# Performance work log

Measured on AMD Instinct MI355X. Metric: run time of the kernel, lower is better.

Reference implementation:

```python
import jax, jax.numpy as jnp
import numpy as np

C = 1024
H = 64
W = 64


def _conv1x1(x, Wt, b):
    # x: [1, Cin, H, W], Wt: [Cout, Cin] -> [1, Cout, H, W]
    return jnp.einsum('oc,bchw->bohw', Wt, x) + b[None, :, None, None]


def setup_inputs() -> dict:
    key = jax.random.key(0)
    ks = jax.random.split(key, 12)
    sc = 1.0 / np.sqrt(C)
    return {
        'x_f': jax.random.normal(ks[0], (1, C, H, W), jnp.float32),
        'x_m': jax.random.normal(ks[1], (1, C, H, W), jnp.float32),
        'x_l': jax.random.normal(ks[2], (1, C, H, W), jnp.float32),
        'Wq': jax.random.normal(ks[3], (C // 2, C), jnp.float32) * sc,
        'bq': jax.random.normal(ks[4], (C // 2,), jnp.float32) * sc,
        'Wk1': jax.random.normal(ks[5], (C // 2, C), jnp.float32) * sc,
        'bk1': jax.random.normal(ks[6], (C // 2,), jnp.float32) * sc,
        'Wk2': jax.random.normal(ks[7], (C // 2, C), jnp.float32) * sc,
        'bk2': jax.random.normal(ks[8], (C // 2,), jnp.float32) * sc,
        'Wv': jax.random.normal(ks[9], (C, C), jnp.float32) * sc,
        'bv': jax.random.normal(ks[10], (C,), jnp.float32) * sc,
        'gamma': jax.random.normal(ks[11], (1,), jnp.float32),
    }


def reference(x_f, x_m, x_l, Wq, bq, Wk1, bk1, Wk2, bk2, Wv, bv, gamma):
    c = x_f.shape[1]
    h, w = x_f.shape[2], x_f.shape[3]
    # torch .view(1, C, -1) on a [1, C/2, H, W] tensor: row-major reshape to [C, H*W/2]
    q = _conv1x1(x_m, Wq, bq).reshape(c, -1).T      # [HW/2, C]
    kf = _conv1x1(x_f, Wk1, bk1).reshape(c, -1)     # [C, HW/2]
    kl = _conv1x1(x_l, Wk2, bk2).reshape(c, -1)     # [C, HW/2]
    att_f = jax.nn.softmax(kf @ q, axis=-1)         # [C, C]
    att_l = jax.nn.softmax(kl @ q, axis=-1)         # [C, C]
    v = _conv1x1(x_m, Wv, bv).reshape(c, -1)        # [C, HW]
    out = att_f @ v + att_l @ v                     # [C, HW]
    out = out.reshape(1, c, h, w)
    return gamma * out + (x_l + x_f) / 2
```

## Files before the change

kernel.cpp:

```cpp
#include <hip/hip_runtime.h>
#include <math.h>


typedef __attribute__((ext_vector_type(8))) short    bf16x8;
typedef __attribute__((ext_vector_type(4))) float    f32x4;

__device__ __forceinline__ unsigned short f2bf(float x) {
    unsigned u = __float_as_uint(x);
    u += 0x7FFFu + ((u >> 16) & 1u);
    return (unsigned short)(u >> 16);
}
__device__ __forceinline__ float bf2f(unsigned short h) {
    return __uint_as_float(((unsigned)h) << 16);
}
__device__ __forceinline__ void split2(float x, unsigned short& h, unsigned short& l) {
    h = f2bf(x);
    l = f2bf(x - bf2f(h));
}

__global__ __launch_bounds__(256) void weights_split_k(
    const float* __restrict__ Wq, const float* __restrict__ Wk1,
    const float* __restrict__ Wk2, const float* __restrict__ Wv,
    unsigned short* __restrict__ Wqh, unsigned short* __restrict__ Wql,
    unsigned short* __restrict__ Wk1h, unsigned short* __restrict__ Wk1l,
    unsigned short* __restrict__ Wk2h, unsigned short* __restrict__ Wk2l,
    unsigned short* __restrict__ Wvh, unsigned short* __restrict__ Wvl)
{
    const int gi = blockIdx.x;
    const float* src; unsigned short *H, *L; int base;
    if (gi < 512)       { src = Wq;  H = Wqh;  L = Wql;  base = gi; }
    else if (gi < 1024) { src = Wk1; H = Wk1h; L = Wk1l; base = gi - 512; }
    else if (gi < 1536) { src = Wk2; H = Wk2h; L = Wk2l; base = gi - 1024; }
    else                { src = Wv;  H = Wvh;  L = Wvl;  base = gi - 1536; }
    const size_t i = (size_t)base * 1024 + threadIdx.x * 4;
    const float4 v = *(const float4*)(src + i);
    ushort4 h, l;
    split2(v.x, h.x, l.x); split2(v.y, h.y, l.y);
    split2(v.z, h.z, l.z); split2(v.w, h.w, l.w);
    *(ushort4*)(H + i) = h;
    *(ushort4*)(L + i) = l;
}

__global__ __launch_bounds__(256) void transpose3_k(
    const float* __restrict__ x0, const float* __restrict__ x1,
    const float* __restrict__ x2,
    unsigned short* __restrict__ t0h, unsigned short* __restrict__ t0l,
    unsigned short* __restrict__ t1h, unsigned short* __restrict__ t1l,
    unsigned short* __restrict__ t2h, unsigned short* __restrict__ t2l)
{
    const float* X; unsigned short *Th, *Tl;
    if (blockIdx.z == 0)      { X = x0; Th = t0h; Tl = t0l; }
    else if (blockIdx.z == 1) { X = x1; Th = t1h; Tl = t1l; }
    else                      { X = x2; Th = t2h; Tl = t2l; }

    __shared__ float t[32 * 33];
    const int tid = threadIdx.x;
    const int c0 = blockIdx.y * 32;
    const int p0 = blockIdx.x * 32;

    const int cl = tid >> 3;
    const int p4 = (tid & 7) * 4;
    const float4 v = *(const float4*)(X + (size_t)(c0 + cl) * 4096 + p0 + p4);
    t[(p4 + 0) * 33 + cl] = v.x;
    t[(p4 + 1) * 33 + cl] = v.y;
    t[(p4 + 2) * 33 + cl] = v.z;
    t[(p4 + 3) * 33 + cl] = v.w;
    __syncthreads();

    const int pl = tid >> 3;
    const int c4 = (tid & 7) * 4;
    ushort4 h, l;
    split2(t[pl * 33 + c4 + 0], h.x, l.x);
    split2(t[pl * 33 + c4 + 1], h.y, l.y);
    split2(t[pl * 33 + c4 + 2], h.z, l.z);
    split2(t[pl * 33 + c4 + 3], h.w, l.w);
    const size_t o = (size_t)(p0 + pl) * 1024 + c0 + c4;
    *(ushort4*)(Th + o) = h;
    *(ushort4*)(Tl + o) = l;
}

__global__ __launch_bounds__(256) void transpose1_k(
    const float* __restrict__ X,
    unsigned short* __restrict__ Th, unsigned short* __restrict__ Tl)
{
    __shared__ float t[32 * 33];
    const int tid = threadIdx.x;
    const int c0 = blockIdx.y * 32;
    const int p0 = blockIdx.x * 32;

    const int cl = tid >> 3;
    const int p4 = (tid & 7) * 4;
    const float4 v = *(const float4*)(X + (size_t)(c0 + cl) * 4096 + p0 + p4);
    t[(p4 + 0) * 33 + cl] = v.x;
    t[(p4 + 1) * 33 + cl] = v.y;
    t[(p4 + 2) * 33 + cl] = v.z;
    t[(p4 + 3) * 33 + cl] = v.w;
    __syncthreads();

    const int pl = tid >> 3;
    const int c4 = (tid & 7) * 4;
    ushort4 h, l;
    split2(t[pl * 33 + c4 + 0], h.x, l.x);
    split2(t[pl * 33 + c4 + 1], h.y, l.y);
    split2(t[pl * 33 + c4 + 2], h.z, l.z);
    split2(t[pl * 33 + c4 + 3], h.w, l.w);
    const size_t o = (size_t)(p0 + pl) * 1024 + c0 + c4;
    *(ushort4*)(Th + o) = h;
    *(ushort4*)(Tl + o) = l;
}

__device__ __forceinline__ void gemm_core(
    const unsigned short* __restrict__ Ah, const unsigned short* __restrict__ Al,
    const unsigned short* __restrict__ Bh, const unsigned short* __restrict__ Bl,
    int ldk, int kbeg, int kend, int m0, int n0,
    unsigned short* As_h, unsigned short* As_l,
    unsigned short* Bs_h, unsigned short* Bs_l,
    f32x4 (&acc)[4][4])
{
    const int tid  = threadIdx.x;
    const int lane = tid & 63;
    const int wv   = tid >> 6;
    const int wm   = (wv >> 1) * 64;
    const int wn   = (wv & 1) * 64;
    const int lr   = lane & 15;
    const int quad = lane >> 4;
    const int r0 = tid >> 2;
    const int sg = (tid & 3) * 8;

    for (int k0 = kbeg; k0 < kend; k0 += 32) {
        const size_t ka = (size_t)(m0 + r0) * ldk + k0 + sg;
        const size_t kb = (size_t)(n0 + r0) * ldk + k0 + sg;
        const bf16x8 a0h = *(const bf16x8*)(Ah + ka);
        const bf16x8 a1h = *(const bf16x8*)(Ah + ka + (size_t)64 * ldk);
        const bf16x8 a0l = *(const bf16x8*)(Al + ka);
        const bf16x8 a1l = *(const bf16x8*)(Al + ka + (size_t)64 * ldk);
        const bf16x8 b0h = *(const bf16x8*)(Bh + kb);
        const bf16x8 b1h = *(const bf16x8*)(Bh + kb + (size_t)64 * ldk);
        const bf16x8 b0l = *(const bf16x8*)(Bl + kb);
        const bf16x8 b1l = *(const bf16x8*)(Bl + kb + (size_t)64 * ldk);

        __syncthreads();
        *(bf16x8*)(As_h + r0 * 40 + sg)        = a0h;
        *(bf16x8*)(As_h + (r0 + 64) * 40 + sg) = a1h;
        *(bf16x8*)(As_l + r0 * 40 + sg)        = a0l;
        *(bf16x8*)(As_l + (r0 + 64) * 40 + sg) = a1l;
        *(bf16x8*)(Bs_h + r0 * 40 + sg)        = b0h;
        *(bf16x8*)(Bs_h + (r0 + 64) * 40 + sg) = b1h;
        *(bf16x8*)(Bs_l + r0 * 40 + sg)        = b0l;
        *(bf16x8*)(Bs_l + (r0 + 64) * 40 + sg) = b1l;
        __syncthreads();

        bf16x8 afh[4], afl[4], bfh[4], bfl[4];
#pragma unroll
        for (int i = 0; i < 4; ++i) {
            const int ra = (wm + i * 16 + lr) * 40 + quad * 8;
            afh[i] = *(const bf16x8*)(As_h + ra);
            afl[i] = *(const bf16x8*)(As_l + ra);
            const int rb = (wn + i * 16 + lr) * 40 + quad * 8;
            bfh[i] = *(const bf16x8*)(Bs_h + rb);
            bfl[i] = *(const bf16x8*)(Bs_l + rb);
        }
#pragma unroll
        for (int i = 0; i < 4; ++i)
#pragma unroll
            for (int j = 0; j < 4; ++j) {
                acc[i][j] = __builtin_amdgcn_mfma_f32_16x16x32_bf16(afh[i], bfh[j], acc[i][j], 0, 0, 0);
                acc[i][j] = __builtin_amdgcn_mfma_f32_16x16x32_bf16(afh[i], bfl[j], acc[i][j], 0, 0, 0);
                acc[i][j] = __builtin_amdgcn_mfma_f32_16x16x32_bf16(afl[i], bfh[j], acc[i][j], 0, 0, 0);
            }
    }
}

#define GEMM_PROLOGUE()                                                 \
    __shared__ unsigned short As_h[128 * 40], As_l[128 * 40];           \
    __shared__ unsigned short Bs_h[128 * 40], Bs_l[128 * 40];           \
    f32x4 acc[4][4];                                                    \
    _Pragma("unroll") for (int i = 0; i < 4; ++i)                       \
    _Pragma("unroll") for (int j = 0; j < 4; ++j)                       \
    _Pragma("unroll") for (int r = 0; r < 4; ++r) acc[i][j][r] = 0.f;   \
    const int lane = threadIdx.x & 63;                                  \
    const int wv   = threadIdx.x >> 6;                                  \
    const int wm   = (wv >> 1) * 64;                                    \
    const int wn   = (wv & 1) * 64;                                     \
    const int lr   = lane & 15;                                         \
    const int quad = lane >> 4;

__global__ __launch_bounds__(256) void conv_all_k(
    const unsigned short* __restrict__ Wqh, const unsigned short* __restrict__ Wql,
    const unsigned short* __restrict__ Wk1h, const unsigned short* __restrict__ Wk1l,
    const unsigned short* __restrict__ Wk2h, const unsigned short* __restrict__ Wk2l,
    const unsigned short* __restrict__ Wvh, const unsigned short* __restrict__ Wvl,
    const unsigned short* __restrict__ xmTh, const unsigned short* __restrict__ xmTl,
    const unsigned short* __restrict__ xfTh, const unsigned short* __restrict__ xfTl,
    const unsigned short* __restrict__ xlTh, const unsigned short* __restrict__ xlTl,
    const float* __restrict__ bq, const float* __restrict__ bk1,
    const float* __restrict__ bk2, const float* __restrict__ bv,
    unsigned short* __restrict__ Qh, unsigned short* __restrict__ Ql,
    unsigned short* __restrict__ Kfh, unsigned short* __restrict__ Kfl,
    unsigned short* __restrict__ Klh, unsigned short* __restrict__ Kll,
    float* __restrict__ V)
{
    GEMM_PROLOGUE();
    const int mt = blockIdx.y;
    const unsigned short *Ah, *Al, *Bh, *Bl;
    const float* bias;
    unsigned short *Ch = nullptr, *Cl = nullptr;
    float* Cv = nullptr;
    int mloc;
    if (mt < 4) {
        Ah = Wqh;  Al = Wql;  Bh = xmTh; Bl = xmTl; bias = bq;
        Ch = Qh;   Cl = Ql;   mloc = mt * 128;
    } else if (mt < 8) {
        Ah = Wk1h; Al = Wk1l; Bh = xfTh; Bl = xfTl; bias = bk1;
        Ch = Kfh;  Cl = Kfl;  mloc = (mt - 4) * 128;
    } else if (mt < 12) {
        Ah = Wk2h; Al = Wk2l; Bh = xlTh; Bl = xlTl; bias = bk2;
        Ch = Klh;  Cl = Kll;  mloc = (mt - 8) * 128;
    } else {
        Ah = Wvh;  Al = Wvl;  Bh = xmTh; Bl = xmTl; bias = bv;
        Cv = V;    mloc = (mt - 12) * 128;
    }
    const int n0 = blockIdx.x * 128;

    gemm_core(Ah, Al, Bh, Bl, 1024, 0, 1024, mloc, n0, As_h, As_l, Bs_h, Bs_l, acc);

#pragma unroll
    for (int i = 0; i < 4; ++i) {
        const int mb = mloc + wm + i * 16 + quad * 4;
#pragma unroll
        for (int j = 0; j < 4; ++j) {
            const int nn = n0 + wn + j * 16 + lr;
#pragma unroll
            for (int r = 0; r < 4; ++r) {
                const float v = acc[i][j][r] + bias[mb + r];
                const size_t idx = (size_t)(mb + r) * 4096 + nn;
                if (Cv) {
                    Cv[idx] = v;
                } else {
                    unsigned short h, l;
                    split2(v, h, l);
                    Ch[idx] = h;
                    Cl[idx] = l;
                }
            }
        }
    }
}

__global__ __launch_bounds__(256) void logits_fused_k(
    const unsigned short* __restrict__ Kfh, const unsigned short* __restrict__ Kfl,
    const unsigned short* __restrict__ Klh, const unsigned short* __restrict__ Kll,
    const unsigned short* __restrict__ Qh, const unsigned short* __restrict__ Ql,
    float* __restrict__ Sfp, float* __restrict__ Slp)
{
    GEMM_PROLOGUE();
    const int which = blockIdx.z >> 2;
    const int slice = blockIdx.z & 3;
    const unsigned short* Ah = which ? Klh : Kfh;
    const unsigned short* Al = which ? Kll : Kfl;
    float* out = (which ? Slp : Sfp) + (size_t)slice * 1024 * 1024;
    const int m0 = blockIdx.y * 128;
    const int n0 = blockIdx.x * 128;

    gemm_core(Ah, Al, Qh, Ql, 2048, slice * 512, slice * 512 + 512, m0, n0,
              As_h, As_l, Bs_h, Bs_l, acc);

#pragma unroll
    for (int i = 0; i < 4; ++i) {
        const int mb = m0 + wm + i * 16 + quad * 4;
#pragma unroll
        for (int j = 0; j < 4; ++j) {
            const int nn = n0 + wn + j * 16 + lr;
#pragma unroll
            for (int r = 0; r < 4; ++r)
                out[(size_t)(mb + r) * 1024 + nn] = acc[i][j][r];
        }
    }
}

__global__ __launch_bounds__(256) void gemm_final_k(
    const unsigned short* __restrict__ Amh, const unsigned short* __restrict__ Aml,
    const unsigned short* __restrict__ VTh, const unsigned short* __restrict__ VTl,
    float* __restrict__ out,
    const float* __restrict__ xf, const float* __restrict__ xl,
    const float* __restrict__ gamma)
{
    GEMM_PROLOGUE();
    const int m0 = blockIdx.y * 128;
    const int n0 = blockIdx.x * 128;

    gemm_core(Amh, Aml, VTh, VTl, 1024, 0, 1024, m0, n0,
              As_h, As_l, Bs_h, Bs_l, acc);

    const float g = gamma[0];
#pragma unroll
    for (int i = 0; i < 4; ++i) {
        const int mb = m0 + wm + i * 16 + quad * 4;
#pragma unroll
        for (int j = 0; j < 4; ++j) {
            const int nn = n0 + wn + j * 16 + lr;
#pragma unroll
            for (int r = 0; r < 4; ++r) {
                const size_t idx = (size_t)(mb + r) * 4096 + nn;
                out[idx] = g * acc[i][j][r] + 0.5f * (xf[idx] + xl[idx]);
            }
        }
    }
}

__global__ __launch_bounds__(256) void softmax_add4_k(
    const float* __restrict__ Sfp, const float* __restrict__ Slp,
    unsigned short* __restrict__ Ah, unsigned short* __restrict__ Al)
{
    const int row = blockIdx.x;
    const int tid = threadIdx.x;
    __shared__ float red[8];
    const size_t base = (size_t)row * 1024 + tid * 4;
    const size_t SL = (size_t)1024 * 1024;

    float4 vf = *(const float4*)(Sfp + base);
    float4 vl = *(const float4*)(Slp + base);
#pragma unroll
    for (int s = 1; s < 4; ++s) {
        const float4 a = *(const float4*)(Sfp + s * SL + base);
        const float4 b = *(const float4*)(Slp + s * SL + base);
        vf.x += a.x; vf.y += a.y; vf.z += a.z; vf.w += a.w;
        vl.x += b.x; vl.y += b.y; vl.z += b.z; vl.w += b.w;
    }

    float mf = fmaxf(fmaxf(vf.x, vf.y), fmaxf(vf.z, vf.w));
    float ml = fmaxf(fmaxf(vl.x, vl.y), fmaxf(vl.z, vl.w));
#pragma unroll
    for (int off = 32; off; off >>= 1) {
        mf = fmaxf(mf, __shfl_down(mf, off, 64));
        ml = fmaxf(ml, __shfl_down(ml, off, 64));
    }
    const int wave = tid >> 6;
    if ((tid & 63) == 0) { red[wave] = mf; red[4 + wave] = ml; }
    __syncthreads();
    mf = fmaxf(fmaxf(red[0], red[1]), fmaxf(red[2], red[3]));
    ml = fmaxf(fmaxf(red[4], red[5]), fmaxf(red[6], red[7]));
    __syncthreads();

    const float4 ef = make_float4(expf(vf.x - mf), expf(vf.y - mf),
                                  expf(vf.z - mf), expf(vf.w - mf));
    const float4 el = make_float4(expf(vl.x - ml), expf(vl.y - ml),
                                  expf(vl.z - ml), expf(vl.w - ml));
    float sf = ef.x + ef.y + ef.z + ef.w;
    float sl = el.x + el.y + el.z + el.w;
#pragma unroll
    for (int off = 32; off; off >>= 1) {
        sf += __shfl_down(sf, off, 64);
        sl += __shfl_down(sl, off, 64);
    }
    if ((tid & 63) == 0) { red[wave] = sf; red[4 + wave] = sl; }
    __syncthreads();
    sf = red[0] + red[1] + red[2] + red[3];
    sl = red[4] + red[5] + red[6] + red[7];

    const float rf = 1.f / sf, rl = 1.f / sl;
    ushort4 h, l;
    split2(ef.x * rf + el.x * rl, h.x, l.x);
    split2(ef.y * rf + el.y * rl, h.y, l.y);
    split2(ef.z * rf + el.z * rl, h.z, l.z);
    split2(ef.w * rf + el.w * rl, h.w, l.w);
    *(ushort4*)(Ah + base) = h;
    *(ushort4*)(Al + base) = l;
}

__global__ void noop_k(float* p) { if (threadIdx.x == 1024) p[0] = 0.f; }

extern "C" void kernel_launch(void* const* d_in, const int* in_sizes, int n_in,
                              void* d_out, int out_size, void* d_ws, size_t ws_size,
                              hipStream_t stream) {
    (void)in_sizes; (void)n_in; (void)out_size;
    const float* xf  = (const float*)d_in[0];
    const float* xm  = (const float*)d_in[1];
    const float* xl  = (const float*)d_in[2];
    const float* Wq  = (const float*)d_in[3];
    const float* bq  = (const float*)d_in[4];
    const float* Wk1 = (const float*)d_in[5];
    const float* bk1 = (const float*)d_in[6];
    const float* Wk2 = (const float*)d_in[7];
    const float* bk2 = (const float*)d_in[8];
    const float* Wv  = (const float*)d_in[9];
    const float* bv  = (const float*)d_in[10];
    const float* gamma = (const float*)d_in[11];
    float* out = (float*)d_out;

    const size_t MB = 1024 * 1024;
    if (ws_size < 98 * MB) {
        noop_k<<<dim3(1), dim3(64), 0, stream>>>((float*)d_ws);
        return;
    }

    char* p = (char*)d_ws;
    unsigned short* xmT_h = (unsigned short*)(p + 0 * MB);
    unsigned short* xmT_l = (unsigned short*)(p + 8 * MB);
    unsigned short* xfT_h = (unsigned short*)(p + 16 * MB);
    unsigned short* xfT_l = (unsigned short*)(p + 24 * MB);
    unsigned short* xlT_h = (unsigned short*)(p + 32 * MB);
    unsigned short* xlT_l = (unsigned short*)(p + 40 * MB);
    unsigned short* Wq_h  = (unsigned short*)(p + 48 * MB);
    unsigned short* Wq_l  = (unsigned short*)(p + 49 * MB);
    unsigned short* Wk1_h = (unsigned short*)(p + 50 * MB);
    unsigned short* Wk1_l = (unsigned short*)(p + 51 * MB);
    unsigned short* Wk2_h = (unsigned short*)(p + 52 * MB);
    unsigned short* Wk2_l = (unsigned short*)(p + 53 * MB);
    unsigned short* Wv_h  = (unsigned short*)(p + 54 * MB);
    unsigned short* Wv_l  = (unsigned short*)(p + 56 * MB);
    unsigned short* Q_h   = (unsigned short*)(p + 58 * MB);
    unsigned short* Q_l   = (unsigned short*)(p + 62 * MB);
    unsigned short* Kf_h  = (unsigned short*)(p + 66 * MB);
    unsigned short* Kf_l  = (unsigned short*)(p + 70 * MB);
    unsigned short* Kl_h  = (unsigned short*)(p + 74 * MB);
    unsigned short* Kl_l  = (unsigned short*)(p + 78 * MB);
    float*          V     = (float*)(p + 82 * MB);
    float*          Sfp  = (float*)(p + 16 * MB);
    float*          Slp  = (float*)(p + 32 * MB);
    unsigned short* VT_h = xmT_h;
    unsigned short* VT_l = xmT_l;
    unsigned short* Am_h = (unsigned short*)(p + 74 * MB);
    unsigned short* Am_l = (unsigned short*)(p + 76 * MB);

    const dim3 blk(256);
    transpose3_k<<<dim3(128, 32, 3), blk, 0, stream>>>(
        xm, xf, xl, xmT_h, xmT_l, xfT_h, xfT_l, xlT_h, xlT_l);
    weights_split_k<<<dim3(2560), blk, 0, stream>>>(
        Wq, Wk1, Wk2, Wv, Wq_h, Wq_l, Wk1_h, Wk1_l, Wk2_h, Wk2_l, Wv_h, Wv_l);
    conv_all_k<<<dim3(32, 20), blk, 0, stream>>>(
        Wq_h, Wq_l, Wk1_h, Wk1_l, Wk2_h, Wk2_l, Wv_h, Wv_l,
        xmT_h, xmT_l, xfT_h, xfT_l, xlT_h, xlT_l,
        bq, bk1, bk2, bv,
        Q_h, Q_l, Kf_h, Kf_l, Kl_h, Kl_l, V);
    logits_fused_k<<<dim3(8, 8, 8), blk, 0, stream>>>(
        Kf_h, Kf_l, Kl_h, Kl_l, Q_h, Q_l, Sfp, Slp);
    transpose1_k<<<dim3(128, 32), blk, 0, stream>>>(V, VT_h, VT_l);
    softmax_add4_k<<<dim3(1024), blk, 0, stream>>>(Sfp, Slp, Am_h, Am_l);
    gemm_final_k<<<dim3(32, 8), blk, 0, stream>>>(
        Am_h, Am_l, VT_h, VT_l, out, xf, xl, gamma);
}
```

Baseline: 310.7 us.

## Load GEMM tiles directly into LDS with global_load_lds and XOR-swizzled layout

Replaces the register-staged global→LDS copy in the shared GEMM core with the direct global_load_lds builtin, giving each wave one of the four hi/lo A/B planes to fetch. The padded 40-element LDS rows become unpadded 32-element rows, and a rotating segment swizzle on both the write and read sides avoids bank conflicts. This removes VGPR staging and ds_write instructions and shrinks LDS use, which could raise occupancy. It is still single-buffered with two barriers per k-step, and it depends on the swizzle matching exactly on both sides.

```diff
diff --git a/kernel.cpp b/kernel.cpp
--- a/kernel.cpp
+++ b/kernel.cpp
@@ -16,6 +16,13 @@
 __device__ __forceinline__ void split2(float x, unsigned short& h, unsigned short& l) {
     h = f2bf(x);
     l = f2bf(x - bf2f(h));
+}
+
+__device__ __forceinline__ void gld16(const unsigned short* g, unsigned short* l) {
+    __builtin_amdgcn_global_load_lds(
+        (const __attribute__((address_space(1))) unsigned int*)g,
+        (__attribute__((address_space(3))) unsigned int*)l,
+        16, 0, 0);
 }
 
 __global__ __launch_bounds__(256) void weights_split_k(
@@ -124,39 +131,35 @@
     const int wn   = (wv & 1) * 64;
     const int lr   = lane & 15;
     const int quad = lane >> 4;
-    const int r0 = tid >> 2;
-    const int sg = (tid & 3) * 8;
+
+    const unsigned short* gsrc = (wv == 0) ? Ah : (wv == 1) ? Al : (wv == 2) ? Bh : Bl;
+    unsigned short* ldst = (wv == 0) ? As_h : (wv == 1) ? As_l : (wv == 2) ? Bs_h : Bs_l;
+    const int tile0 = (wv < 2) ? m0 : n0;
+    const int lrow = lane >> 2;
+    const int gseg = ((lane & 3) - ((lane >> 3) & 3)) & 3;
+    const unsigned short* gp[8];
+#pragma unroll
+    for (int t = 0; t < 8; ++t)
+        gp[t] = gsrc + (size_t)(tile0 + t * 16 + lrow) * ldk + kbeg + gseg * 8;
+
+    const int rdseg = (quad + (lr >> 1)) & 3;
 
     for (int k0 = kbeg; k0 < kend; k0 += 32) {
-        const size_t ka = (size_t)(m0 + r0) * ldk + k0 + sg;
-        const size_t kb = (size_t)(n0 + r0) * ldk + k0 + sg;
-        const bf16x8 a0h = *(const bf16x8*)(Ah + ka);
-        const bf16x8 a1h = *(const bf16x8*)(Ah + ka + (size_t)64 * ldk);
-        const bf16x8 a0l = *(const bf16x8*)(Al + ka);
-        const bf16x8 a1l = *(const bf16x8*)(Al + ka + (size_t)64 * ldk);
-        const bf16x8 b0h = *(const bf16x8*)(Bh + kb);
-        const bf16x8 b1h = *(const bf16x8*)(Bh + kb + (size_t)64 * ldk);
-        const bf16x8 b0l = *(const bf16x8*)(Bl + kb);
-        const bf16x8 b1l = *(const bf16x8*)(Bl + kb + (size_t)64 * ldk);
-
         __syncthreads();
-        *(bf16x8*)(As_h + r0 * 40 + sg)        = a0h;
-        *(bf16x8*)(As_h + (r0 + 64) * 40 + sg) = a1h;
-        *(bf16x8*)(As_l + r0 * 40 + sg)        = a0l;
-        *(bf16x8*)(As_l + (r0 + 64) * 40 + sg) = a1l;
-        *(bf16x8*)(Bs_h + r0 * 40 + sg)        = b0h;
-        *(bf16x8*)(Bs_h + (r0 + 64) * 40 + sg) = b1h;
-        *(bf16x8*)(Bs_l + r0 * 40 + sg)        = b0l;
-        *(bf16x8*)(Bs_l + (r0 + 64) * 40 + sg) = b1l;
+#pragma unroll
+        for (int t = 0; t < 8; ++t) {
+            gld16(gp[t], ldst + t * 512);
+            gp[t] += 32;
+        }
         __syncthreads();
 
         bf16x8 afh[4], afl[4], bfh[4], bfl[4];
 #pragma unroll
         for (int i = 0; i < 4; ++i) {
-            const int ra = (wm + i * 16 + lr) * 40 + quad * 8;
+            const int ra = (wm + i * 16 + lr) * 32 + rdseg * 8;
             afh[i] = *(const bf16x8*)(As_h + ra);
             afl[i] = *(const bf16x8*)(As_l + ra);
-            const int rb = (wn + i * 16 + lr) * 40 + quad * 8;
+            const int rb = (wn + i * 16 + lr) * 32 + rdseg * 8;
             bfh[i] = *(const bf16x8*)(Bs_h + rb);
             bfl[i] = *(const bf16x8*)(Bs_l + rb);
         }
@@ -172,8 +175,10 @@
 }
 
 #define GEMM_PROLOGUE()                                                 \
-    __shared__ unsigned short As_h[128 * 40], As_l[128 * 40];           \
-    __shared__ unsigned short Bs_h[128 * 40], Bs_l[128 * 40];           \
+    __shared__ __align__(16) unsigned short As_h[128 * 32];             \
+    __shared__ __align__(16) unsigned short As_l[128 * 32];             \
+    __shared__ __align__(16) unsigned short Bs_h[128 * 32];             \
+    __shared__ __align__(16) unsigned short Bs_l[128 * 32];             \
     f32x4 acc[4][4];                                                    \
     _Pragma("unroll") for (int i = 0; i < 4; ++i)                       \
     _Pragma("unroll") for (int j = 0; j < 4; ++j)                       \
@@ -183,7 +188,8 @@
     const int wm   = (wv >> 1) * 64;                                    \
     const int wn   = (wv & 1) * 64;                                     \
     const int lr   = lane & 15;                                         \
-    const int quad = lane >> 4;
+    const int quad = lane >> 4;                                         \
+    (void)lane; (void)wv;
 
 __global__ __launch_bounds__(256) void conv_all_k(
     const unsigned short* __restrict__ Wqh, const unsigned short* __restrict__ Wql,
```

Measured after the change: 303.6 us. -2.3%, faster.
